# Kernel tuning notes

Measured on AMD Instinct MI355X. Metric: run time of the kernel, lower is better.

## Reference

```python
import jax, jax.numpy as jnp
import numpy as np

N, T, V, C = 64, 64, 64, 64   # batch, time(=ref_channels), joints(=kpt_channels), in_channels
RED, OUT = 2, 64              # red_channels, out_channels


def setup_inputs() -> dict:
    key = jax.random.key(0)
    ks = jax.random.split(key, 8)
    s_m = (2.0 / C) ** 0.5          # kaiming-ish scale for 1x1 convs
    s_rm = (2.0 / (RED * T)) ** 0.5
    s_f = (1.0 / C) ** 0.5
    return {
        "x": jax.random.normal(ks[0], (N, T, V, C), dtype=jnp.float32),
        "A": jax.random.normal(ks[1], (T, V, V), dtype=jnp.float32) * 0.1,
        "w_m1": jax.random.normal(ks[2], (RED, C), dtype=jnp.float32) * s_m,
        "b_m1": jnp.zeros((RED,), dtype=jnp.float32),
        "w_m2": jax.random.normal(ks[3], (RED, C), dtype=jnp.float32) * s_m,
        "b_m2": jnp.zeros((RED,), dtype=jnp.float32),
        "w_rm": jax.random.normal(ks[4], (T, RED * T), dtype=jnp.float32) * s_rm,
        "b_rm": jnp.zeros((T,), dtype=jnp.float32),
        "w_f": jax.random.normal(ks[5], (OUT, C), dtype=jnp.float32) * s_f,
        "b_f": jnp.zeros((OUT,), dtype=jnp.float32),
        "alpha_m": 1,
    }


def reference(x, A, w_m1, b_m1, w_m2, b_m2, w_rm, b_rm, w_f, b_f, alpha_m):
    n = x.shape[0]
    # conv_f: pointwise Linear over channels -> (N,T,V,OUT)
    xf = jnp.einsum('ntvc,oc->ntvo', x, w_f) + b_f
    # conv_m1/conv_m2: 1x1 Conv2d over channel dim -> (N,RED,T,V)
    xm1 = jnp.einsum('ntvc,rc->nrtv', x, w_m1) + b_m1[None, :, None, None]
    xm2 = jnp.einsum('ntvc,rc->nrtv', x, w_m2) + b_m2[None, :, None, None]
    xm1 = xm1.reshape(n, RED * T, V)
    xm2 = xm2.reshape(n, RED * T, V)
    # pairwise outer difference + tanh -> (N, RED*T, V, V)
    xm = jnp.tanh(xm1[..., :, None] - xm2[..., None, :])
    # conv_rm: 1x1 conv reducing RED*T -> T channels, then scale + static adjacency
    adj = jnp.einsum('nkij,tk->ntij', xm, w_rm) + b_rm[None, :, None, None]
    adj = adj * alpha_m + A[None]          # (N,T,V,V)
    # batched matmul: dynamic adjacency x features
    out = jnp.einsum('ntij,ntjo->ntio', adj, xf)  # (N,T,V,OUT)
    return out
```

## Files before the change

### kernel.cpp

```cpp
#include <hip/hip_runtime.h>
#include <hip/hip_bf16.h>


typedef float  f32x4  __attribute__((ext_vector_type(4)));
typedef short  bf16x8 __attribute__((ext_vector_type(8)));
typedef short  bf16x4 __attribute__((ext_vector_type(4)));

static __device__ __forceinline__ short f2bf(float f) {
    __hip_bfloat16 h = __float2bfloat16(f);
    return *reinterpret_cast<short*>(&h);
}

static __device__ __forceinline__ float bf2f(short s) {
    return __uint_as_float(((unsigned)(unsigned short)s) << 16);
}

static __device__ __forceinline__ bf16x8 cvt8f(const float4 a, const float4 b) {
    bf16x8 r;
    r[0] = f2bf(a.x); r[1] = f2bf(a.y); r[2] = f2bf(a.z); r[3] = f2bf(a.w);
    r[4] = f2bf(b.x); r[5] = f2bf(b.y); r[6] = f2bf(b.z); r[7] = f2bf(b.w);
    return r;
}

static __device__ __forceinline__ bf16x8 cvt8(const float* p) {
    return cvt8f(*(const float4*)p, *(const float4*)(p + 4));
}

static __device__ __forceinline__ float tanh_fast(float x) {
    float e = __expf(2.0f * x);
    return 1.0f - 2.0f * __builtin_amdgcn_rcpf(e + 1.0f);
}

static __device__ __forceinline__ float dot4(float4 a, float4 b) {
    return a.x * b.x + a.y * b.y + a.z * b.z + a.w * b.w;
}

static __device__ __forceinline__ float alpha_decode(const int* p) {
    int raw = p[0];
    unsigned ur = (unsigned)(raw < 0 ? -raw : raw);
    return (ur < (1u << 23)) ? (float)raw : __int_as_float(raw);
}

#define MFMA16(a, b, c) __builtin_amdgcn_mfma_f32_16x16x32_bf16((a), (b), (c), 0, 0, 0)

__global__ __launch_bounds__(512) void k0_stream2(
    const float* __restrict__ x,
    const float* __restrict__ w_m1, const float* __restrict__ b_m1,
    const float* __restrict__ w_m2, const float* __restrict__ b_m2,
    short* __restrict__ xbf, float* __restrict__ m1T, float* __restrict__ m2T)
{
    __shared__ float msT[4][8][68];

    const int b   = blockIdx.x;
    const int n   = b >> 3;
    const int v0  = (b & 7) * 8;
    const int tid = threadIdx.x;
    const int tl  = tid >> 6;
    const int vv  = (tid >> 3) & 7;
    const int cg  = tid & 7;
    const int c0  = cg * 8;

    const float4 w10 = *(const float4*)(w_m1 + c0);
    const float4 w11 = *(const float4*)(w_m1 + c0 + 4);
    const float4 w20 = *(const float4*)(w_m1 + 64 + c0);
    const float4 w21 = *(const float4*)(w_m1 + 64 + c0 + 4);
    const float4 w30 = *(const float4*)(w_m2 + c0);
    const float4 w31 = *(const float4*)(w_m2 + c0 + 4);
    const float4 w40 = *(const float4*)(w_m2 + 64 + c0);
    const float4 w41 = *(const float4*)(w_m2 + 64 + c0 + 4);

#pragma unroll 2
    for (int it = 0; it < 8; ++it) {
        const int t = it * 8 + tl;
        const size_t R = ((size_t)(n * 64 + t)) * 64 + (v0 + vv);
        const float* xp = x + (R << 6) + c0;
        const float4 a0 = *(const float4*)xp;
        const float4 a1 = *(const float4*)(xp + 4);

        float s0 = dot4(a0, w10) + dot4(a1, w11);
        float s1 = dot4(a0, w20) + dot4(a1, w21);
        float s2 = dot4(a0, w30) + dot4(a1, w31);
        float s3 = dot4(a0, w40) + dot4(a1, w41);

        *(bf16x8*)(xbf + (R << 6) + c0) = cvt8f(a0, a1);

#pragma unroll
        for (int m = 1; m < 8; m <<= 1) {
            s0 += __shfl_xor(s0, m);
            s1 += __shfl_xor(s1, m);
            s2 += __shfl_xor(s2, m);
            s3 += __shfl_xor(s3, m);
        }
        if (cg < 4) {
            float s = (cg == 0) ? s0 : (cg == 1) ? s1 : (cg == 2) ? s2 : s3;
            msT[cg][vv][t] = s;
        }
    }
    __syncthreads();

    {
        const int m   = tid >> 8;
        const int rem = tid & 255;
        const int vv2 = rem >> 5;
        const int k0  = (rem & 31) * 4;
        const int r   = k0 >> 6;
        const int sel = m * 2 + r;
        const int t0  = k0 & 63;
        float4 val = *(const float4*)&msT[sel][vv2][t0];
        const float bias = (m == 0) ? b_m1[r] : b_m2[r];
        val.x += bias; val.y += bias; val.z += bias; val.w += bias;
        float* dst = ((m == 0) ? m1T : m2T) + n * 8192 + (v0 + vv2) * 128 + k0;
        *(float4*)dst = val;
    }
}

__global__ __launch_bounds__(512) void k1_adj(
    const float* __restrict__ w_rm,
    const float* __restrict__ m1T,  const float* __restrict__ m2T,
    const int* __restrict__ alpha_p,
    short* __restrict__ adjm)
{
    __shared__ float m2s[64 * 132];
    __shared__ short wrs[64 * 132];

    const int b   = blockIdx.x;
    const int n   = b >> 3;
    const int i0  = (b & 7) * 8;
    const int tid = threadIdx.x;

    const float alpha = alpha_decode(alpha_p);

    {
        const float4* src = (const float4*)(m2T + n * 8192);
        for (int it = tid; it < 2048; it += 512) {
            int j = it >> 5, q = it & 31;
            *(float4*)(m2s + j * 132 + q * 4) = src[it];
        }
    }
    {
        const float4* src = (const float4*)w_rm;
        for (int it = tid; it < 2048; it += 512) {
            int t = it >> 5, q = it & 31;
            float4 v = src[it];
            bf16x4 pv;
            pv[0] = f2bf(alpha * v.x);
            pv[1] = f2bf(alpha * v.y);
            pv[2] = f2bf(alpha * v.z);
            pv[3] = f2bf(alpha * v.w);
            *(bf16x4*)(wrs + t * 132 + q * 4) = pv;
        }
    }
    __syncthreads();

    const int l = tid & 63, w = tid >> 6;
    const int lr = l & 15, lg = l >> 4;
    const int ig = i0 + w;

    float4 m1r[8];
#pragma unroll
    for (int kt = 0; kt < 4; ++kt) {
        const float* p = m1T + n * 8192 + ig * 128 + kt * 32 + lg * 8;
        m1r[kt * 2 + 0] = *(const float4*)p;
        m1r[kt * 2 + 1] = *(const float4*)(p + 4);
    }

    short* adjb = adjm + ((size_t)n << 18) + (ig << 6);

#pragma unroll 1
    for (int jt = 0; jt < 4; ++jt) {
        const float* m2row = m2s + (jt * 16 + lr) * 132;
        bf16x8 bfr[4];
#pragma unroll
        for (int kt = 0; kt < 4; ++kt) {
            const int k0 = kt * 32 + lg * 8;
            float4 b0 = *(const float4*)(m2row + k0);
            float4 b1 = *(const float4*)(m2row + k0 + 4);
            float4 a0 = m1r[kt * 2], a1 = m1r[kt * 2 + 1];
            bfr[kt][0] = f2bf(tanh_fast(a0.x - b0.x));
            bfr[kt][1] = f2bf(tanh_fast(a0.y - b0.y));
            bfr[kt][2] = f2bf(tanh_fast(a0.z - b0.z));
            bfr[kt][3] = f2bf(tanh_fast(a0.w - b0.w));
            bfr[kt][4] = f2bf(tanh_fast(a1.x - b1.x));
            bfr[kt][5] = f2bf(tanh_fast(a1.y - b1.y));
            bfr[kt][6] = f2bf(tanh_fast(a1.z - b1.z));
            bfr[kt][7] = f2bf(tanh_fast(a1.w - b1.w));
        }

        const int j0 = jt * 16 + lg * 4;
#pragma unroll
        for (int q = 0; q < 4; ++q) {
            const int tq = q * 16 + lr;
            bf16x8 af[4];
#pragma unroll
            for (int kt = 0; kt < 4; ++kt)
                af[kt] = *(const bf16x8*)(wrs + tq * 132 + kt * 32 + lg * 8);
            f32x4 acc = (f32x4){0.f, 0.f, 0.f, 0.f};
#pragma unroll
            for (int kt = 0; kt < 4; ++kt)
                acc = MFMA16(bfr[kt], af[kt], acc);
            bf16x4 pv;
            pv[0] = f2bf(acc[0]);
            pv[1] = f2bf(acc[1]);
            pv[2] = f2bf(acc[2]);
            pv[3] = f2bf(acc[3]);
            *(bf16x4*)(adjb + ((size_t)tq << 12) + j0) = pv;
        }
    }
}

__global__ __launch_bounds__(256) void k2_out(
    const short* __restrict__ adjm, const short* __restrict__ xbf,
    const float* __restrict__ Ast,  const float* __restrict__ b_rm,
    const int* __restrict__ alpha_p,
    const float* __restrict__ w_f,  const float* __restrict__ b_f,
    float* __restrict__ out)
{
    __shared__ short adjs[64 * 72];
    __shared__ short xT[64 * 72 + 32];
    __shared__ short P[64 * 104];

    const int pair = blockIdx.x;
    const int t    = pair & 63;
    const int tid  = threadIdx.x;
    const int l = tid & 63, w = tid >> 6;
    const int lr = l & 15, lg = l >> 4;

    const short* Ab = adjm + ((size_t)pair << 12);
    const short* Xb = xbf  + ((size_t)pair << 12);
    const float* At = Ast  + ((size_t)t << 12);
    float*       Ob = out  + ((size_t)pair << 12);

    const float ab = alpha_decode(alpha_p) * b_rm[t];

#pragma unroll
    for (int pass = 0; pass < 2; ++pass) {
        const int it  = pass * 256 + tid;
        const int row = it >> 3;
        const int c8  = (it & 7) * 8;
        bf16x8 s  = *(const bf16x8*)(Ab + row * 64 + c8);
        float4 a0 = *(const float4*)(At + row * 64 + c8);
        float4 a1 = *(const float4*)(At + row * 64 + c8 + 4);
        bf16x8 r;
        r[0] = f2bf(bf2f(s[0]) + a0.x + ab);
        r[1] = f2bf(bf2f(s[1]) + a0.y + ab);
        r[2] = f2bf(bf2f(s[2]) + a0.z + ab);
        r[3] = f2bf(bf2f(s[3]) + a0.w + ab);
        r[4] = f2bf(bf2f(s[4]) + a1.x + ab);
        r[5] = f2bf(bf2f(s[5]) + a1.y + ab);
        r[6] = f2bf(bf2f(s[6]) + a1.z + ab);
        r[7] = f2bf(bf2f(s[7]) + a1.w + ab);
        *(bf16x8*)(adjs + row * 72 + c8) = r;
    }

    {
        const int j  = tid >> 2;
        const int c0 = (tid & 3) * 16;
        bf16x8 r0 = *(const bf16x8*)(Xb + j * 64 + c0);
        bf16x8 r1 = *(const bf16x8*)(Xb + j * 64 + c0 + 8);
        const int g0 = (c0 >> 4) * 8;
#pragma unroll
        for (int d = 0; d < 8; ++d) {
            xT[(c0 + d) * 72 + g0 + j]     = r0[d];
            xT[(c0 + 8 + d) * 72 + g0 + j] = r1[d];
        }
    }
    if (tid < 128) {
        int row = tid >> 1, cz = 80 + (tid & 1) * 8;
        bf16x8 z = {0, 0, 0, 0, 0, 0, 0, 0};
        *(bf16x8*)(P + row * 104 + cz) = z;
    }
    __syncthreads();

    bf16x8 adjA[4][2];
#pragma unroll
    for (int mt = 0; mt < 4; ++mt)
#pragma unroll
        for (int ks = 0; ks < 2; ++ks)
            adjA[mt][ks] = *(const bf16x8*)(adjs + (mt * 16 + lr) * 72
                                            + ks * 32 + lg * 8);

    {
        bf16x8 bx[2];
#pragma unroll
        for (int ks = 0; ks < 2; ++ks)
            bx[ks] = *(const bf16x8*)(xT + (w * 16 + lr) * 72 + w * 8
                                      + ks * 32 + lg * 8);

        f32x4 acc[4];
#pragma unroll
        for (int mt = 0; mt < 4; ++mt) acc[mt] = (f32x4){0.f, 0.f, 0.f, 0.f};
#pragma unroll
        for (int ks = 0; ks < 2; ++ks)
#pragma unroll
            for (int mt = 0; mt < 4; ++mt)
                acc[mt] = MFMA16(adjA[mt][ks], bx[ks], acc[mt]);

#pragma unroll
        for (int mt = 0; mt < 4; ++mt)
#pragma unroll
            for (int e = 0; e < 4; ++e)
                P[(mt * 16 + lg * 4 + e) * 104 + w * 16 + lr] = f2bf(acc[mt][e]);

        if (w == 0) {
            bf16x8 ones = {0, 0, 0, 0, 0, 0, 0, 0};
            if (lr == 0) {
#pragma unroll
                for (int d = 0; d < 8; ++d) ones[d] = (short)0x3F80;
            }
            f32x4 accO[4];
#pragma unroll
            for (int mt = 0; mt < 4; ++mt) accO[mt] = (f32x4){0.f, 0.f, 0.f, 0.f};
#pragma unroll
            for (int ks = 0; ks < 2; ++ks)
#pragma unroll
                for (int mt = 0; mt < 4; ++mt)
                    accO[mt] = MFMA16(adjA[mt][ks], ones, accO[mt]);
#pragma unroll
            for (int mt = 0; mt < 4; ++mt)
#pragma unroll
                for (int e = 0; e < 4; ++e)
                    P[(mt * 16 + lg * 4 + e) * 104 + 64 + lr] = f2bf(accO[mt][e]);
        }
    }
    __syncthreads();

    {
        const int o = w * 16 + lr;
        bf16x8 afw[3];
#pragma unroll
        for (int ks = 0; ks < 2; ++ks)
            afw[ks] = cvt8(w_f + o * 64 + ks * 32 + lg * 8);
        {
            bf16x8 ab2 = {0, 0, 0, 0, 0, 0, 0, 0};
            if (lg == 0) ab2[0] = f2bf(b_f[o]);
            afw[2] = ab2;
        }

#pragma unroll
        for (int nt = 0; nt < 4; ++nt) {
            const int i = nt * 16 + lr;
            bf16x8 bP[3];
#pragma unroll
            for (int ks = 0; ks < 3; ++ks)
                bP[ks] = *(const bf16x8*)(P + i * 104 + ks * 32 + lg * 8);
            f32x4 acc = (f32x4){0.f, 0.f, 0.f, 0.f};
#pragma unroll
            for (int ks = 0; ks < 3; ++ks)
                acc = MFMA16(afw[ks], bP[ks], acc);
            *(f32x4*)(Ob + i * 64 + w * 16 + lg * 4) = acc;
        }
    }
}

extern "C" void kernel_launch(void* const* d_in, const int* in_sizes, int n_in,
                              void* d_out, int out_size, void* d_ws, size_t ws_size,
                              hipStream_t stream)
{
    const float* x    = (const float*)d_in[0];
    const float* A    = (const float*)d_in[1];
    const float* w_m1 = (const float*)d_in[2];
    const float* b_m1 = (const float*)d_in[3];
    const float* w_m2 = (const float*)d_in[4];
    const float* b_m2 = (const float*)d_in[5];
    const float* w_rm = (const float*)d_in[6];
    const float* b_rm = (const float*)d_in[7];
    const float* w_f  = (const float*)d_in[8];
    const float* b_f  = (const float*)d_in[9];
    const int*   alpha = (const int*)d_in[10];

    char* ws = (char*)d_ws;
    short* adjm = (short*)(ws);
    short* xbf = (short*)(ws + (size_t)34 * 1024 * 1024);
    float* m1T = (float*)(ws + (size_t)66 * 1024 * 1024);
    float* m2T = (float*)(ws + (size_t)68 * 1024 * 1024);
    float* out = (float*)d_out;

    k0_stream2<<<dim3(512), dim3(512), 0, stream>>>(x, w_m1, b_m1, w_m2, b_m2,
                                                    xbf, m1T, m2T);
    k1_adj<<<dim3(512), dim3(512), 0, stream>>>(w_rm, m1T, m2T, alpha, adjm);
    k2_out<<<dim3(4096), dim3(256), 0, stream>>>(adjm, xbf, A, b_rm, alpha,
                                                 w_f, b_f, out);
}
```

Baseline: 70.47 us.

## Process two (n,t) pairs per k2 block with software-prefetched second pair

```diff
diff --git a/kernel.cpp b/kernel.cpp
--- a/kernel.cpp
+++ b/kernel.cpp
@@ -39,6 +39,20 @@
     int raw = p[0];
     unsigned ur = (unsigned)(raw < 0 ? -raw : raw);
     return (ur < (1u << 23)) ? (float)raw : __int_as_float(raw);
+}
+
+static __device__ __forceinline__ bf16x8 fuse8(bf16x8 s, float4 a0, float4 a1,
+                                               float ab) {
+    bf16x8 r;
+    r[0] = f2bf(bf2f(s[0]) + a0.x + ab);
+    r[1] = f2bf(bf2f(s[1]) + a0.y + ab);
+    r[2] = f2bf(bf2f(s[2]) + a0.z + ab);
+    r[3] = f2bf(bf2f(s[3]) + a0.w + ab);
+    r[4] = f2bf(bf2f(s[4]) + a1.x + ab);
+    r[5] = f2bf(bf2f(s[5]) + a1.y + ab);
+    r[6] = f2bf(bf2f(s[6]) + a1.z + ab);
+    r[7] = f2bf(bf2f(s[7]) + a1.w + ab);
+    return r;
 }
 
 #define MFMA16(a, b, c) __builtin_amdgcn_mfma_f32_16x16x32_bf16((a), (b), (c), 0, 0, 0)
@@ -219,73 +233,94 @@
     __shared__ short xT[64 * 72 + 32];
     __shared__ short P[64 * 104];
 
-    const int pair = blockIdx.x;
-    const int t    = pair & 63;
-    const int tid  = threadIdx.x;
+    const int b   = blockIdx.x;
+    const int tid = threadIdx.x;
     const int l = tid & 63, w = tid >> 6;
     const int lr = l & 15, lg = l >> 4;
 
-    const short* Ab = adjm + ((size_t)pair << 12);
-    const short* Xb = xbf  + ((size_t)pair << 12);
-    const float* At = Ast  + ((size_t)t << 12);
-    float*       Ob = out  + ((size_t)pair << 12);
-
-    const float ab = alpha_decode(alpha_p) * b_rm[t];
-
-#pragma unroll
-    for (int pass = 0; pass < 2; ++pass) {
-        const int it  = pass * 256 + tid;
-        const int row = it >> 3;
-        const int c8  = (it & 7) * 8;
-        bf16x8 s  = *(const bf16x8*)(Ab + row * 64 + c8);
-        float4 a0 = *(const float4*)(At + row * 64 + c8);
-        float4 a1 = *(const float4*)(At + row * 64 + c8 + 4);
-        bf16x8 r;
-        r[0] = f2bf(bf2f(s[0]) + a0.x + ab);
-        r[1] = f2bf(bf2f(s[1]) + a0.y + ab);
-        r[2] = f2bf(bf2f(s[2]) + a0.z + ab);
-        r[3] = f2bf(bf2f(s[3]) + a0.w + ab);
-        r[4] = f2bf(bf2f(s[4]) + a1.x + ab);
-        r[5] = f2bf(bf2f(s[5]) + a1.y + ab);
-        r[6] = f2bf(bf2f(s[6]) + a1.z + ab);
-        r[7] = f2bf(bf2f(s[7]) + a1.w + ab);
-        *(bf16x8*)(adjs + row * 72 + c8) = r;
-    }
-
-    {
-        const int j  = tid >> 2;
-        const int c0 = (tid & 3) * 16;
-        bf16x8 r0 = *(const bf16x8*)(Xb + j * 64 + c0);
-        bf16x8 r1 = *(const bf16x8*)(Xb + j * 64 + c0 + 8);
-        const int g0 = (c0 >> 4) * 8;
+    const float alpha = alpha_decode(alpha_p);
+
+    const int row0 = tid >> 3;
+    const int row1 = row0 + 32;
+    const int c8   = (tid & 7) * 8;
+    const int jx   = tid >> 2;
+    const int cx0  = (tid & 3) * 16;
+    const int gx0  = (cx0 >> 4) * 8;
+
+    const int p0 = 2 * b,      p1 = 2 * b + 1;
+    const int t0 = p0 & 63,    t1 = p1 & 63;
+
+    const int o = w * 16 + lr;
+    bf16x8 afw[3];
+#pragma unroll
+    for (int ks = 0; ks < 2; ++ks)
+        afw[ks] = cvt8(w_f + o * 64 + ks * 32 + lg * 8);
+    {
+        bf16x8 ab2 = {0, 0, 0, 0, 0, 0, 0, 0};
+        if (lg == 0) ab2[0] = f2bf(b_f[o]);
+        afw[2] = ab2;
+    }
+    bf16x8 ones = {0, 0, 0, 0, 0, 0, 0, 0};
+    if (lr == 0) {
+#pragma unroll
+        for (int d = 0; d < 8; ++d) ones[d] = (short)0x3F80;
+    }
+
+    {
+        const short* Ab = adjm + ((size_t)p0 << 12);
+        const float* At = Ast  + ((size_t)t0 << 12);
+        const short* Xb = xbf  + ((size_t)p0 << 12);
+        bf16x8 sA  = *(const bf16x8*)(Ab + row0 * 64 + c8);
+        float4 aA0 = *(const float4*)(At + row0 * 64 + c8);
+        float4 aA1 = *(const float4*)(At + row0 * 64 + c8 + 4);
+        bf16x8 sB  = *(const bf16x8*)(Ab + row1 * 64 + c8);
+        float4 aB0 = *(const float4*)(At + row1 * 64 + c8);
+        float4 aB1 = *(const float4*)(At + row1 * 64 + c8 + 4);
+        bf16x8 xrA = *(const bf16x8*)(Xb + jx * 64 + cx0);
+        bf16x8 xrB = *(const bf16x8*)(Xb + jx * 64 + cx0 + 8);
+        const float ab0 = alpha * b_rm[t0];
+
+        *(bf16x8*)(adjs + row0 * 72 + c8) = fuse8(sA, aA0, aA1, ab0);
+        *(bf16x8*)(adjs + row1 * 72 + c8) = fuse8(sB, aB0, aB1, ab0);
 #pragma unroll
         for (int d = 0; d < 8; ++d) {
-            xT[(c0 + d) * 72 + g0 + j]     = r0[d];
-            xT[(c0 + 8 + d) * 72 + g0 + j] = r1[d];
-        }
-    }
-    if (tid < 128) {
-        int row = tid >> 1, cz = 80 + (tid & 1) * 8;
-        bf16x8 z = {0, 0, 0, 0, 0, 0, 0, 0};
-        *(bf16x8*)(P + row * 104 + cz) = z;
-    }
-    __syncthreads();
-
-    bf16x8 adjA[4][2];
+            xT[(cx0 + d) * 72 + gx0 + jx]     = xrA[d];
+            xT[(cx0 + 8 + d) * 72 + gx0 + jx] = xrB[d];
+        }
+        if (tid < 128) {
+            int row = tid >> 1, cz = 80 + (tid & 1) * 8;
+            bf16x8 z = {0, 0, 0, 0, 0, 0, 0, 0};
+            *(bf16x8*)(P + row * 104 + cz) = z;
+        }
+    }
+    __syncthreads();
+
+    bf16x8 adjA[4][2], bx[2];
 #pragma unroll
     for (int mt = 0; mt < 4; ++mt)
 #pragma unroll
         for (int ks = 0; ks < 2; ++ks)
             adjA[mt][ks] = *(const bf16x8*)(adjs + (mt * 16 + lr) * 72
                                             + ks * 32 + lg * 8);
-
-    {
-        bf16x8 bx[2];
-#pragma unroll
-        for (int ks = 0; ks < 2; ++ks)
-            bx[ks] = *(const bf16x8*)(xT + (w * 16 + lr) * 72 + w * 8
-                                      + ks * 32 + lg * 8);
-
+#pragma unroll
+    for (int ks = 0; ks < 2; ++ks)
+        bx[ks] = *(const bf16x8*)(xT + (w * 16 + lr) * 72 + w * 8
+                                  + ks * 32 + lg * 8);
+
+    const short* Ab1 = adjm + ((size_t)p1 << 12);
+    const float* At1 = Ast  + ((size_t)t1 << 12);
+    const short* Xb1 = xbf  + ((size_t)p1 << 12);
+    bf16x8 sA1  = *(const bf16x8*)(Ab1 + row0 * 64 + c8);
+    float4 aA01 = *(const float4*)(At1 + row0 * 64 + c8);
+    float4 aA11 = *(const float4*)(At1 + row0 * 64 + c8 + 4);
+    bf16x8 sB1  = *(const bf16x8*)(Ab1 + row1 * 64 + c8);
+    float4 aB01 = *(const float4*)(At1 + row1 * 64 + c8);
+    float4 aB11 = *(const float4*)(At1 + row1 * 64 + c8 + 4);
+    bf16x8 xrA1 = *(const bf16x8*)(Xb1 + jx * 64 + cx0);
+    bf16x8 xrB1 = *(const bf16x8*)(Xb1 + jx * 64 + cx0 + 8);
+    const float ab1 = alpha * b_rm[t1];
+
+    {
         f32x4 acc[4];
 #pragma unroll
         for (int mt = 0; mt < 4; ++mt) acc[mt] = (f32x4){0.f, 0.f, 0.f, 0.f};
@@ -294,19 +329,12 @@
 #pragma unroll
             for (int mt = 0; mt < 4; ++mt)
                 acc[mt] = MFMA16(adjA[mt][ks], bx[ks], acc[mt]);
-
 #pragma unroll
         for (int mt = 0; mt < 4; ++mt)
 #pragma unroll
             for (int e = 0; e < 4; ++e)
                 P[(mt * 16 + lg * 4 + e) * 104 + w * 16 + lr] = f2bf(acc[mt][e]);
-
         if (w == 0) {
-            bf16x8 ones = {0, 0, 0, 0, 0, 0, 0, 0};
-            if (lr == 0) {
-#pragma unroll
-                for (int d = 0; d < 8; ++d) ones[d] = (short)0x3F80;
-            }
             f32x4 accO[4];
 #pragma unroll
             for (int mt = 0; mt < 4; ++mt) accO[mt] = (f32x4){0.f, 0.f, 0.f, 0.f};
@@ -325,17 +353,75 @@
     __syncthreads();
 
     {
-        const int o = w * 16 + lr;
-        bf16x8 afw[3];
+        float* Ob = out + ((size_t)p0 << 12);
+#pragma unroll
+        for (int nt = 0; nt < 4; ++nt) {
+            const int i = nt * 16 + lr;
+            bf16x8 bP[3];
+#pragma unroll
+            for (int ks = 0; ks < 3; ++ks)
+                bP[ks] = *(const bf16x8*)(P + i * 104 + ks * 32 + lg * 8);
+            f32x4 acc = (f32x4){0.f, 0.f, 0.f, 0.f};
+#pragma unroll
+            for (int ks = 0; ks < 3; ++ks)
+                acc = MFMA16(afw[ks], bP[ks], acc);
+            *(f32x4*)(Ob + i * 64 + w * 16 + lg * 4) = acc;
+        }
+    }
+    *(bf16x8*)(adjs + row0 * 72 + c8) = fuse8(sA1, aA01, aA11, ab1);
+    *(bf16x8*)(adjs + row1 * 72 + c8) = fuse8(sB1, aB01, aB11, ab1);
+#pragma unroll
+    for (int d = 0; d < 8; ++d) {
+        xT[(cx0 + d) * 72 + gx0 + jx]     = xrA1[d];
+        xT[(cx0 + 8 + d) * 72 + gx0 + jx] = xrB1[d];
+    }
+    __syncthreads();
+
+#pragma unroll
+    for (int mt = 0; mt < 4; ++mt)
 #pragma unroll
         for (int ks = 0; ks < 2; ++ks)
-            afw[ks] = cvt8(w_f + o * 64 + ks * 32 + lg * 8);
-        {
-            bf16x8 ab2 = {0, 0, 0, 0, 0, 0, 0, 0};
-            if (lg == 0) ab2[0] = f2bf(b_f[o]);
-            afw[2] = ab2;
-        }
-
+            adjA[mt][ks] = *(const bf16x8*)(adjs + (mt * 16 + lr) * 72
+                                            + ks * 32 + lg * 8);
+#pragma unroll
+    for (int ks = 0; ks < 2; ++ks)
+        bx[ks] = *(const bf16x8*)(xT + (w * 16 + lr) * 72 + w * 8
+                                  + ks * 32 + lg * 8);
+
+    {
+        f32x4 acc[4];
+#pragma unroll
+        for (int mt = 0; mt < 4; ++mt) acc[mt] = (f32x4){0.f, 0.f, 0.f, 0.f};
+#pragma unroll
+        for (int ks = 0; ks < 2; ++ks)
+#pragma unroll
+            for (int mt = 0; mt < 4; ++mt)
+                acc[mt] = MFMA16(adjA[mt][ks], bx[ks], acc[mt]);
+#pragma unroll
+        for (int mt = 0; mt < 4; ++mt)
+#pragma unroll
+            for (int e = 0; e < 4; ++e)
+                P[(mt * 16 + lg * 4 + e) * 104 + w * 16 + lr] = f2bf(acc[mt][e]);
+        if (w == 0) {
+            f32x4 accO[4];
+#pragma unroll
+            for (int mt = 0; mt < 4; ++mt) accO[mt] = (f32x4){0.f, 0.f, 0.f, 0.f};
+#pragma unroll
+            for (int ks = 0; ks < 2; ++ks)
+#pragma unroll
+                for (int mt = 0; mt < 4; ++mt)
+                    accO[mt] = MFMA16(adjA[mt][ks], ones, accO[mt]);
+#pragma unroll
+            for (int mt = 0; mt < 4; ++mt)
+#pragma unroll
+                for (int e = 0; e < 4; ++e)
+                    P[(mt * 16 + lg * 4 + e) * 104 + 64 + lr] = f2bf(accO[mt][e]);
+        }
+    }
+    __syncthreads();
+
+    {
+        float* Ob = out + ((size_t)p1 << 12);
 #pragma unroll
         for (int nt = 0; nt < 4; ++nt) {
             const int i = nt * 16 + lr;
@@ -378,6 +464,6 @@
     k0_stream2<<<dim3(512), dim3(512), 0, stream>>>(x, w_m1, b_m1, w_m2, b_m2,
                                                     xbf, m1T, m2T);
     k1_adj<<<dim3(512), dim3(512), 0, stream>>>(w_rm, m1T, m2T, alpha, adjm);
-    k2_out<<<dim3(4096), dim3(256), 0, stream>>>(adjm, xbf, A, b_rm, alpha,
+    k2_out<<<dim3(2048), dim3(256), 0, stream>>>(adjm, xbf, A, b_rm, alpha,
                                                  w_f, b_f, out);
 }
```

New measurement: 68.92 us. -2.2%, faster.

## Process four pairs per block in k2 with register-prefetched next tile

Applied to the files above, without the earlier changes.

```diff
diff --git a/kernel.cpp b/kernel.cpp
--- a/kernel.cpp
+++ b/kernel.cpp
@@ -39,6 +39,20 @@
     int raw = p[0];
     unsigned ur = (unsigned)(raw < 0 ? -raw : raw);
     return (ur < (1u << 23)) ? (float)raw : __int_as_float(raw);
+}
+
+static __device__ __forceinline__ bf16x8 fuse8(bf16x8 s, float4 a0, float4 a1,
+                                               float ab) {
+    bf16x8 r;
+    r[0] = f2bf(bf2f(s[0]) + a0.x + ab);
+    r[1] = f2bf(bf2f(s[1]) + a0.y + ab);
+    r[2] = f2bf(bf2f(s[2]) + a0.z + ab);
+    r[3] = f2bf(bf2f(s[3]) + a0.w + ab);
+    r[4] = f2bf(bf2f(s[4]) + a1.x + ab);
+    r[5] = f2bf(bf2f(s[5]) + a1.y + ab);
+    r[6] = f2bf(bf2f(s[6]) + a1.z + ab);
+    r[7] = f2bf(bf2f(s[7]) + a1.w + ab);
+    return r;
 }
 
 #define MFMA16(a, b, c) __builtin_amdgcn_mfma_f32_16x16x32_bf16((a), (b), (c), 0, 0, 0)
@@ -127,8 +141,19 @@
     const int n   = b >> 3;
     const int i0  = (b & 7) * 8;
     const int tid = threadIdx.x;
+    const int l = tid & 63, w = tid >> 6;
+    const int lr = l & 15, lg = l >> 4;
+    const int ig = i0 + w;
 
     const float alpha = alpha_decode(alpha_p);
+
+    float4 m1r[8];
+#pragma unroll
+    for (int kt = 0; kt < 4; ++kt) {
+        const float* p = m1T + n * 8192 + ig * 128 + kt * 32 + lg * 8;
+        m1r[kt * 2 + 0] = *(const float4*)p;
+        m1r[kt * 2 + 1] = *(const float4*)(p + 4);
+    }
 
     {
         const float4* src = (const float4*)(m2T + n * 8192);
@@ -151,18 +176,6 @@
         }
     }
     __syncthreads();
-
-    const int l = tid & 63, w = tid >> 6;
-    const int lr = l & 15, lg = l >> 4;
-    const int ig = i0 + w;
-
-    float4 m1r[8];
-#pragma unroll
-    for (int kt = 0; kt < 4; ++kt) {
-        const float* p = m1T + n * 8192 + ig * 128 + kt * 32 + lg * 8;
-        m1r[kt * 2 + 0] = *(const float4*)p;
-        m1r[kt * 2 + 1] = *(const float4*)(p + 4);
-    }
 
     short* adjb = adjm + ((size_t)n << 18) + (ig << 6);
 
@@ -219,50 +232,61 @@
     __shared__ short xT[64 * 72 + 32];
     __shared__ short P[64 * 104];
 
-    const int pair = blockIdx.x;
-    const int t    = pair & 63;
-    const int tid  = threadIdx.x;
+    const int b   = blockIdx.x;
+    const int tid = threadIdx.x;
     const int l = tid & 63, w = tid >> 6;
     const int lr = l & 15, lg = l >> 4;
 
-    const short* Ab = adjm + ((size_t)pair << 12);
-    const short* Xb = xbf  + ((size_t)pair << 12);
-    const float* At = Ast  + ((size_t)t << 12);
-    float*       Ob = out  + ((size_t)pair << 12);
-
-    const float ab = alpha_decode(alpha_p) * b_rm[t];
-
-#pragma unroll
-    for (int pass = 0; pass < 2; ++pass) {
-        const int it  = pass * 256 + tid;
-        const int row = it >> 3;
-        const int c8  = (it & 7) * 8;
-        bf16x8 s  = *(const bf16x8*)(Ab + row * 64 + c8);
-        float4 a0 = *(const float4*)(At + row * 64 + c8);
-        float4 a1 = *(const float4*)(At + row * 64 + c8 + 4);
-        bf16x8 r;
-        r[0] = f2bf(bf2f(s[0]) + a0.x + ab);
-        r[1] = f2bf(bf2f(s[1]) + a0.y + ab);
-        r[2] = f2bf(bf2f(s[2]) + a0.z + ab);
-        r[3] = f2bf(bf2f(s[3]) + a0.w + ab);
-        r[4] = f2bf(bf2f(s[4]) + a1.x + ab);
-        r[5] = f2bf(bf2f(s[5]) + a1.y + ab);
-        r[6] = f2bf(bf2f(s[6]) + a1.z + ab);
-        r[7] = f2bf(bf2f(s[7]) + a1.w + ab);
-        *(bf16x8*)(adjs + row * 72 + c8) = r;
-    }
-
+    const float alpha = alpha_decode(alpha_p);
+
+    const int row0 = tid >> 3;
+    const int row1 = row0 + 32;
+    const int c8   = (tid & 7) * 8;
+    const int jx   = tid >> 2;
+    const int cx0  = (tid & 3) * 16;
+    const int gx0  = (cx0 >> 4) * 8;
+
+    const int o = w * 16 + lr;
+    bf16x8 afw[3];
+#pragma unroll
+    for (int ks = 0; ks < 2; ++ks)
+        afw[ks] = cvt8(w_f + o * 64 + ks * 32 + lg * 8);
     {
-        const int j  = tid >> 2;
-        const int c0 = (tid & 3) * 16;
-        bf16x8 r0 = *(const bf16x8*)(Xb + j * 64 + c0);
-        bf16x8 r1 = *(const bf16x8*)(Xb + j * 64 + c0 + 8);
-        const int g0 = (c0 >> 4) * 8;
-#pragma unroll
-        for (int d = 0; d < 8; ++d) {
-            xT[(c0 + d) * 72 + g0 + j]     = r0[d];
-            xT[(c0 + 8 + d) * 72 + g0 + j] = r1[d];
-        }
+        bf16x8 ab2 = {0, 0, 0, 0, 0, 0, 0, 0};
+        if (lg == 0) ab2[0] = f2bf(b_f[o]);
+        afw[2] = ab2;
+    }
+    bf16x8 ones = {0, 0, 0, 0, 0, 0, 0, 0};
+    if (lr == 0) {
+#pragma unroll
+        for (int d = 0; d < 8; ++d) ones[d] = (short)0x3F80;
+    }
+
+    bf16x8 sA, sB, xrA, xrB;
+    float4 aA0, aA1, aB0, aB1;
+    float  ab;
+
+    {
+        const int p = 4 * b, t = p & 63;
+        const short* Ab = adjm + ((size_t)p << 12);
+        const float* At = Ast  + ((size_t)t << 12);
+        const short* Xb = xbf  + ((size_t)p << 12);
+        sA  = *(const bf16x8*)(Ab + row0 * 64 + c8);
+        aA0 = *(const float4*)(At + row0 * 64 + c8);
+        aA1 = *(const float4*)(At + row0 * 64 + c8 + 4);
+        sB  = *(const bf16x8*)(Ab + row1 * 64 + c8);
+        aB0 = *(const float4*)(At + row1 * 64 + c8);
+        aB1 = *(const float4*)(At + row1 * 64 + c8 + 4);
+        xrA = *(const bf16x8*)(Xb + jx * 64 + cx0);
+        xrB = *(const bf16x8*)(Xb + jx * 64 + cx0 + 8);
+        ab  = alpha * b_rm[t];
+    }
+    *(bf16x8*)(adjs + row0 * 72 + c8) = fuse8(sA, aA0, aA1, ab);
+    *(bf16x8*)(adjs + row1 * 72 + c8) = fuse8(sB, aB0, aB1, ab);
+#pragma unroll
+    for (int d = 0; d < 8; ++d) {
+        xT[(cx0 + d) * 72 + gx0 + jx]     = xrA[d];
+        xT[(cx0 + 8 + d) * 72 + gx0 + jx] = xrB[d];
     }
     if (tid < 128) {
         int row = tid >> 1, cz = 80 + (tid & 1) * 8;
@@ -271,84 +295,99 @@
     }
     __syncthreads();
 
-    bf16x8 adjA[4][2];
-#pragma unroll
-    for (int mt = 0; mt < 4; ++mt)
-#pragma unroll
-        for (int ks = 0; ks < 2; ++ks)
-            adjA[mt][ks] = *(const bf16x8*)(adjs + (mt * 16 + lr) * 72
-                                            + ks * 32 + lg * 8);
-
-    {
-        bf16x8 bx[2];
+#pragma unroll
+    for (int pp = 0; pp < 4; ++pp) {
+        const int pair = 4 * b + pp;
+
+        bf16x8 adjA[4][2], bx[2];
+#pragma unroll
+        for (int mt = 0; mt < 4; ++mt)
+#pragma unroll
+            for (int ks = 0; ks < 2; ++ks)
+                adjA[mt][ks] = *(const bf16x8*)(adjs + (mt * 16 + lr) * 72
+                                                + ks * 32 + lg * 8);
 #pragma unroll
         for (int ks = 0; ks < 2; ++ks)
             bx[ks] = *(const bf16x8*)(xT + (w * 16 + lr) * 72 + w * 8
                                       + ks * 32 + lg * 8);
 
-        f32x4 acc[4];
-#pragma unroll
-        for (int mt = 0; mt < 4; ++mt) acc[mt] = (f32x4){0.f, 0.f, 0.f, 0.f};
-#pragma unroll
-        for (int ks = 0; ks < 2; ++ks)
+        if (pp < 3) {
+            const int pn = pair + 1, tn = pn & 63;
+            const short* Ab = adjm + ((size_t)pn << 12);
+            const float* At = Ast  + ((size_t)tn << 12);
+            const short* Xb = xbf  + ((size_t)pn << 12);
+            sA  = *(const bf16x8*)(Ab + row0 * 64 + c8);
+            aA0 = *(const float4*)(At + row0 * 64 + c8);
+            aA1 = *(const float4*)(At + row0 * 64 + c8 + 4);
+            sB  = *(const bf16x8*)(Ab + row1 * 64 + c8);
+            aB0 = *(const float4*)(At + row1 * 64 + c8);
+            aB1 = *(const float4*)(At + row1 * 64 + c8 + 4);
+            xrA = *(const bf16x8*)(Xb + jx * 64 + cx0);
+            xrB = *(const bf16x8*)(Xb + jx * 64 + cx0 + 8);
+            ab  = alpha * b_rm[tn];
+        }
+
+        {
+            f32x4 acc[4];
+#pragma unroll
+            for (int mt = 0; mt < 4; ++mt) acc[mt] = (f32x4){0.f, 0.f, 0.f, 0.f};
+#pragma unroll
+            for (int ks = 0; ks < 2; ++ks)
+#pragma unroll
+                for (int mt = 0; mt < 4; ++mt)
+                    acc[mt] = MFMA16(adjA[mt][ks], bx[ks], acc[mt]);
 #pragma unroll
             for (int mt = 0; mt < 4; ++mt)
-                acc[mt] = MFMA16(adjA[mt][ks], bx[ks], acc[mt]);
-
-#pragma unroll
-        for (int mt = 0; mt < 4; ++mt)
-#pragma unroll
-            for (int e = 0; e < 4; ++e)
-                P[(mt * 16 + lg * 4 + e) * 104 + w * 16 + lr] = f2bf(acc[mt][e]);
-
-        if (w == 0) {
-            bf16x8 ones = {0, 0, 0, 0, 0, 0, 0, 0};
-            if (lr == 0) {
-#pragma unroll
-                for (int d = 0; d < 8; ++d) ones[d] = (short)0x3F80;
+#pragma unroll
+                for (int e = 0; e < 4; ++e)
+                    P[(mt * 16 + lg * 4 + e) * 104 + w * 16 + lr] =
+                        f2bf(acc[mt][e]);
+            if (w == 0) {
+                f32x4 accO[4];
+#pragma unroll
+                for (int mt = 0; mt < 4; ++mt)
+                    accO[mt] = (f32x4){0.f, 0.f, 0.f, 0.f};
+#pragma unroll
+                for (int ks = 0; ks < 2; ++ks)
+#pragma unroll
+                    for (int mt = 0; mt < 4; ++mt)
+                        accO[mt] = MFMA16(adjA[mt][ks], ones, accO[mt]);
+#pragma unroll
+                for (int mt = 0; mt < 4; ++mt)
+#pragma unroll
+                    for (int e = 0; e < 4; ++e)
+                        P[(mt * 16 + lg * 4 + e) * 104 + 64 + lr] =
+                            f2bf(accO[mt][e]);
             }
-            f32x4 accO[4];
-#pragma unroll
-            for (int mt = 0; mt < 4; ++mt) accO[mt] = (f32x4){0.f, 0.f, 0.f, 0.f};
-#pragma unroll
-            for (int ks = 0; ks < 2; ++ks)
-#pragma unroll
-                for (int mt = 0; mt < 4; ++mt)
-                    accO[mt] = MFMA16(adjA[mt][ks], ones, accO[mt]);
-#pragma unroll
-            for (int mt = 0; mt < 4; ++mt)
-#pragma unroll
-                for (int e = 0; e < 4; ++e)
-                    P[(mt * 16 + lg * 4 + e) * 104 + 64 + lr] = f2bf(accO[mt][e]);
-        }
-    }
-    __syncthreads();
-
-    {
-        const int o = w * 16 + lr;
-        bf16x8 afw[3];
-#pragma unroll
-        for (int ks = 0; ks < 2; ++ks)
-            afw[ks] = cvt8(w_f + o * 64 + ks * 32 + lg * 8);
+        }
+        __syncthreads();
+
         {
-            bf16x8 ab2 = {0, 0, 0, 0, 0, 0, 0, 0};
-            if (lg == 0) ab2[0] = f2bf(b_f[o]);
-            afw[2] = ab2;
-        }
-
-#pragma unroll
-        for (int nt = 0; nt < 4; ++nt) {
-            const int i = nt * 16 + lr;
-            bf16x8 bP[3];
-#pragma unroll
-            for (int ks = 0; ks < 3; ++ks)
-                bP[ks] = *(const bf16x8*)(P + i * 104 + ks * 32 + lg * 8);
-            f32x4 acc = (f32x4){0.f, 0.f, 0.f, 0.f};
-#pragma unroll
-            for (int ks = 0; ks < 3; ++ks)
-                acc = MFMA16(afw[ks], bP[ks], acc);
-            *(f32x4*)(Ob + i * 64 + w * 16 + lg * 4) = acc;
-        }
+            float* Ob = out + ((size_t)pair << 12);
+#pragma unroll
+            for (int nt = 0; nt < 4; ++nt) {
+                const int i = nt * 16 + lr;
+                bf16x8 bP[3];
+#pragma unroll
+                for (int ks = 0; ks < 3; ++ks)
+                    bP[ks] = *(const bf16x8*)(P + i * 104 + ks * 32 + lg * 8);
+                f32x4 acc = (f32x4){0.f, 0.f, 0.f, 0.f};
+#pragma unroll
+                for (int ks = 0; ks < 3; ++ks)
+                    acc = MFMA16(afw[ks], bP[ks], acc);
+                *(f32x4*)(Ob + i * 64 + w * 16 + lg * 4) = acc;
+            }
+        }
+        if (pp < 3) {
+            *(bf16x8*)(adjs + row0 * 72 + c8) = fuse8(sA, aA0, aA1, ab);
+            *(bf16x8*)(adjs + row1 * 72 + c8) = fuse8(sB, aB0, aB1, ab);
+#pragma unroll
+            for (int d = 0; d < 8; ++d) {
+                xT[(cx0 + d) * 72 + gx0 + jx]     = xrA[d];
+                xT[(cx0 + 8 + d) * 72 + gx0 + jx] = xrB[d];
+            }
+        }
+        __syncthreads();
     }
 }
 
@@ -378,6 +417,6 @@
     k0_stream2<<<dim3(512), dim3(512), 0, stream>>>(x, w_m1, b_m1, w_m2, b_m2,
                                                     xbf, m1T, m2T);
     k1_adj<<<dim3(512), dim3(512), 0, stream>>>(w_rm, m1T, m2T, alpha, adjm);
-    k2_out<<<dim3(4096), dim3(256), 0, stream>>>(adjm, xbf, A, b_rm, alpha,
+    k2_out<<<dim3(1024), dim3(256), 0, stream>>>(adjm, xbf, A, b_rm, alpha,
                                                  w_f, b_f, out);
 }
```

Result: faster. 67.39 us (-4.4%).
